# Optimization experiments

Measured on AMD Instinct MI355X. Metric: run time of the kernel, lower is better.

Reference implementation:

```python
import jax, jax.numpy as jnp
import numpy as np

B, S, DIM, H = 8, 1024, 768, 12
HD = DIM // H  # head_dim = 64
SCALE = HD ** -0.5


def setup_inputs() -> dict:
    key = jax.random.key(0)
    ks = jax.random.split(key, 9)
    std = DIM ** -0.5
    x = jax.random.normal(ks[0], (B, S, DIM), dtype=jnp.float32)
    Wq = jax.random.normal(ks[1], (DIM, DIM), dtype=jnp.float32) * std
    bq = jax.random.normal(ks[2], (DIM,), dtype=jnp.float32) * 0.01
    Wk = jax.random.normal(ks[3], (DIM, DIM), dtype=jnp.float32) * std
    bk = jax.random.normal(ks[4], (DIM,), dtype=jnp.float32) * 0.01
    Wv = jax.random.normal(ks[5], (DIM, DIM), dtype=jnp.float32) * std
    bv = jax.random.normal(ks[6], (DIM,), dtype=jnp.float32) * 0.01
    Wp = jax.random.normal(ks[7], (DIM, DIM), dtype=jnp.float32) * std
    bp = jax.random.normal(ks[8], (DIM,), dtype=jnp.float32) * 0.01
    return {"x": x, "Wq": Wq, "bq": bq, "Wk": Wk, "bk": bk,
            "Wv": Wv, "bv": bv, "Wp": Wp, "bp": bp}


def _split_heads(t):
    # [b, s, (n d)] -> [b, n, s, d]
    b, s, _ = t.shape
    return t.reshape(b, s, H, HD).transpose(0, 2, 1, 3)


def reference(x, Wq, bq, Wk, bk, Wv, bv, Wp, bp):
    q = _split_heads(x @ Wq + bq)
    k = _split_heads(x @ Wk + bk)
    v = _split_heads(x @ Wv + bv)
    attn = jnp.einsum('bnqd,bnkd->bnqk', q, k) * SCALE
    attn = jax.nn.softmax(attn, axis=-1)
    o = jnp.einsum('bnqk,bnkd->bnqd', attn, v)
    o = o.transpose(0, 2, 1, 3).reshape(x.shape[0], x.shape[1], DIM)
    return o @ Wp + bp
```

## Files before the change

kernel.cpp:

```cpp
#include <hip/hip_runtime.h>
#include <hip/hip_bf16.h>
#include <cstdint>

#define B_    8
#define S_    1024
#define DIM_  768
#define H_    12
#define HD_   64
#define QL2S_ 0.1803368801111204f

typedef __attribute__((ext_vector_type(8))) __bf16 bf16x8;
typedef __attribute__((ext_vector_type(4))) float  f32x4;

__device__ __forceinline__ short f2bf(float f) {
  union { float f; uint32_t u; } a;
  a.f = f;
  uint32_t u = a.u;
  uint32_t r = (u + 0x7FFFu + ((u >> 16) & 1u)) >> 16;
  return (short)r;
}

__device__ __forceinline__ float exp2a(float x) {
  float r;
  asm("v_exp_f32 %0, %1\n\ts_nop 1" : "=v"(r) : "v"(x));
  return r;
}

__device__ __forceinline__ uint32_t cvtpk(float a, float b) {
  uint32_t r;
  asm("v_cvt_pk_bf16_f32 %0, %1, %2" : "=v"(r) : "v"(a), "v"(b));
  return r;
}

__device__ __forceinline__ void gll16(const void* g, void* l) {
  __builtin_amdgcn_global_load_lds((const __attribute__((address_space(1))) void*)g,
                                   (__attribute__((address_space(3))) void*)l, 16, 0, 0);
}

__device__ __forceinline__ int swz(int row, int col) {
  return row * 128 + ((((col >> 3) ^ (row & 7)) & 7) << 4) + ((col & 7) << 1);
}

__global__ __launch_bounds__(256) void k_prep(const float* __restrict__ x,
                                              const float* __restrict__ W0,
                                              const float* __restrict__ W1,
                                              const float* __restrict__ W2,
                                              const float* __restrict__ W3,
                                              short* __restrict__ xb,
                                              short* o0, short* o1,
                                              short* o2, short* o3) {
  const int tx = threadIdx.x, ty = threadIdx.y;
  if (blockIdx.z == 4) {
    const int tid = ty * 32 + tx;
    int i = (blockIdx.y * 24 + blockIdx.x) * 256 + tid;
    const int n4 = 8192 * 768 / 4;
    const int nthr = 24 * 24 * 256;
    for (; i < n4; i += nthr) {
      const float4 v = ((const float4*)x)[i];
      short4 o;
      o.x = f2bf(v.x); o.y = f2bf(v.y); o.z = f2bf(v.z); o.w = f2bf(v.w);
      ((short4*)xb)[i] = o;
    }
    return;
  }
  const float* in = blockIdx.z == 0 ? W0 : blockIdx.z == 1 ? W1 : blockIdx.z == 2 ? W2 : W3;
  short* out = blockIdx.z == 0 ? o0 : blockIdx.z == 1 ? o1 : blockIdx.z == 2 ? o2 : o3;
  __shared__ float tile[32][33];
  const int bx = blockIdx.x * 32, by = blockIdx.y * 32;
#pragma unroll
  for (int j = 0; j < 32; j += 8)
    tile[ty + j][tx] = in[(size_t)(by + ty + j) * DIM_ + bx + tx];
  __syncthreads();
#pragma unroll
  for (int j = 0; j < 32; j += 8)
    out[(size_t)(bx + ty + j) * DIM_ + by + tx] = f2bf(tile[tx][ty + j]);
}

template <int MODE, bool QS>
__device__ __forceinline__ void gemm_body(char* smem,
                                          const short* __restrict__ A,
                                          const short* __restrict__ Bt,
                                          const float* __restrict__ bias,
                                          void* __restrict__ out,
                                          int bm, int bn) {
  char* As = smem;
  char* Bs = smem + 32768;
  const int tid = threadIdx.x;
  const int l = tid & 63, w = tid >> 6;
  const int hi = l >> 4, lo = l & 15;
  const int wr = w >> 1, wc = w & 1;

  auto stageA = [&](int ks, int bo) {
#pragma unroll
    for (int i = 0; i < 4; ++i) {
      const int gl = i * 256 + tid;
      const int row = gl >> 3;
      const int g = (gl & 7) ^ (row & 7);
      gll16(A + (size_t)(bm * 128 + row) * DIM_ + ks * 64 + g * 8, As + bo + gl * 16);
    }
  };
  auto stageB = [&](int ks, int bo) {
#pragma unroll
    for (int i = 0; i < 4; ++i) {
      const int gl = i * 256 + tid;
      const int row = gl >> 3;
      const int g = (gl & 7) ^ (row & 7);
      gll16(Bt + (size_t)(bn * 128 + row) * DIM_ + ks * 64 + g * 8, Bs + bo + gl * 16);
    }
  };

  f32x4 acc[4][4];
  const f32x4 zz = {0.f, 0.f, 0.f, 0.f};
#pragma unroll
  for (int m = 0; m < 4; ++m)
#pragma unroll
    for (int n = 0; n < 4; ++n) acc[m][n] = zz;

  stageA(0, 0);
  stageB(0, 0);
  __syncthreads();

  for (int ks = 0; ks < 12; ++ks) {
    const int cu = (ks & 1) << 14;
    if (ks < 11) { stageA(ks + 1, cu ^ 16384); stageB(ks + 1, cu ^ 16384); }
#pragma unroll
    for (int kk = 0; kk < 2; ++kk) {
      bf16x8 a[4], b[4];
#pragma unroll
      for (int m = 0; m < 4; ++m)
        a[m] = *(const bf16x8*)(As + cu + swz(wr * 64 + m * 16 + lo, kk * 32 + hi * 8));
#pragma unroll
      for (int n = 0; n < 4; ++n)
        b[n] = *(const bf16x8*)(Bs + cu + swz(wc * 64 + n * 16 + lo, kk * 32 + hi * 8));
#pragma unroll
      for (int m = 0; m < 4; ++m)
#pragma unroll
        for (int n = 0; n < 4; ++n)
          acc[m][n] = __builtin_amdgcn_mfma_f32_16x16x32_bf16(a[m], b[n], acc[m][n], 0, 0, 0);
    }
    __syncthreads();
  }

#pragma unroll
  for (int m = 0; m < 4; ++m) {
#pragma unroll
    for (int n = 0; n < 4; ++n) {
#pragma unroll
      for (int r = 0; r < 4; ++r) {
        const int R = bm * 128 + wr * 64 + m * 16 + hi * 4 + r;
        const int C = bn * 128 + wc * 64 + n * 16 + lo;
        float v = acc[m][n][r] + bias[MODE == 1 ? R : C];
        if (QS) v *= QL2S_;
        if (MODE == 0) {
          ((short*)out)[((size_t)((R >> 10) * H_ + (C >> 6)) * S_ + (R & 1023)) * HD_ + (C & 63)] = f2bf(v);
        } else if (MODE == 1) {
          ((short*)out)[((size_t)((C >> 10) * H_ + (R >> 6)) * HD_ + (R & 63)) * S_ + (C & 1023)] = f2bf(v);
        } else {
          ((float*)out)[(size_t)R * DIM_ + C] = v;
        }
      }
    }
  }
}

__global__ __launch_bounds__(256, 2) void k_gemm_qkv(const short* __restrict__ xb,
                                                     const short* __restrict__ WqT,
                                                     const short* __restrict__ WkT,
                                                     const short* __restrict__ WvT,
                                                     const float* __restrict__ bq,
                                                     const float* __restrict__ bk,
                                                     const float* __restrict__ bv,
                                                     short* qo, short* ko, short* vo) {
  __shared__ alignas(16) char smem[65536];
  if (blockIdx.z == 0)
    gemm_body<0, true>(smem, xb, WqT, bq, qo, blockIdx.x, blockIdx.y);
  else if (blockIdx.z == 1)
    gemm_body<0, false>(smem, xb, WkT, bk, ko, blockIdx.x, blockIdx.y);
  else
    gemm_body<1, false>(smem, WvT, xb, bv, vo, blockIdx.y, blockIdx.x);
}

__global__ __launch_bounds__(256, 2) void k_gemm_proj(const short* __restrict__ A,
                                                      const short* __restrict__ Bt,
                                                      const float* __restrict__ bias,
                                                      float* out) {
  __shared__ alignas(16) char smem[65536];
  gemm_body<2, false>(smem, A, Bt, bias, out, blockIdx.y, blockIdx.x);
}

__global__ __launch_bounds__(256, 3) void k_attn(const short* __restrict__ qw,
                                                 const short* __restrict__ kw,
                                                 const short* __restrict__ vtw,
                                                 short* __restrict__ ow) {
  __shared__ alignas(16) char smem[49152];
  char* Kb = smem;
  char* Vb = smem + 16384;
  char* Ps = smem + 32768;
  const int tid = threadIdx.x;
  const int l = tid & 63, w = tid >> 6;
  const int hi = l >> 4, lo = l & 15;
  const int qt = blockIdx.x / 96;
  const int bh = blockIdx.x % 96;

  const short* qg = qw  + (size_t)bh * (S_ * HD_) + (qt * 128) * HD_;
  const short* kg = kw  + (size_t)bh * (S_ * HD_);
  const short* vg = vtw + (size_t)bh * (S_ * HD_);

  auto stage = [&](int T, int bufo) {
#pragma unroll
    for (int i = 0; i < 2; ++i) {
      const int gl = i * 256 + tid;
      const int row = gl >> 3;
      const int g = (gl & 7) ^ (row & 7);
      gll16(kg + (T * 64 + row) * 64 + g * 8, Kb + bufo + gl * 16);
    }
#pragma unroll
    for (int i = 0; i < 2; ++i) {
      const int gl = i * 256 + tid;
      const int row = gl >> 3;
      const int g = (gl & 7) ^ (row & 7);
      gll16(vg + row * 1024 + T * 64 + g * 8, Vb + bufo + gl * 16);
    }
  };

  bf16x8 aQ[2][2];
#pragma unroll
  for (int m = 0; m < 2; ++m)
#pragma unroll
    for (int kk = 0; kk < 2; ++kk)
      aQ[m][kk] = *(const bf16x8*)(qg + (w * 32 + m * 16 + lo) * HD_ + kk * 32 + hi * 8);

  f32x4 o_acc[2][4];
  const f32x4 zz = {0.f, 0.f, 0.f, 0.f};
#pragma unroll
  for (int m = 0; m < 2; ++m)
#pragma unroll
    for (int db = 0; db < 4; ++db) o_acc[m][db] = zz;
  float lsum[2] = {0.f, 0.f};

  stage(0, 0);
  __syncthreads();

  for (int t = 0; t < 16; ++t) {
    const int cu = (t & 1) << 13;
    if (t < 15) stage(t + 1, cu ^ 8192);

    f32x4 sacc[2][4];
#pragma unroll
    for (int m = 0; m < 2; ++m)
#pragma unroll
      for (int nb = 0; nb < 4; ++nb) sacc[m][nb] = zz;
    __builtin_amdgcn_s_setprio(1);
#pragma unroll
    for (int kk = 0; kk < 2; ++kk) {
#pragma unroll
      for (int nb = 0; nb < 4; ++nb) {
        const bf16x8 bK = *(const bf16x8*)(Kb + cu + swz(nb * 16 + lo, kk * 32 + hi * 8));
#pragma unroll
        for (int m = 0; m < 2; ++m)
          sacc[m][nb] = __builtin_amdgcn_mfma_f32_16x16x32_bf16(bK, aQ[m][kk], sacc[m][nb], 0, 0, 0);
      }
    }
    __builtin_amdgcn_s_setprio(0);

#pragma unroll
    for (int m = 0; m < 2; ++m) {
#pragma unroll
      for (int nb = 0; nb < 4; ++nb) {
        const float p0 = exp2a(sacc[m][nb][0] - 1.0f);
        const float p1 = exp2a(sacc[m][nb][1] - 1.0f);
        const float p2 = exp2a(sacc[m][nb][2] - 1.0f);
        const float p3 = exp2a(sacc[m][nb][3] - 1.0f);
        lsum[m] += (p0 + p1) + (p2 + p3);
        uint2 pk;
        pk.x = cvtpk(p0, p1);
        pk.y = cvtpk(p2, p3);
        *(uint2*)(Ps + swz(w * 32 + m * 16 + lo, nb * 16 + hi * 4)) = pk;
      }
    }
    asm volatile("s_waitcnt lgkmcnt(0)" ::: "memory");
    __builtin_amdgcn_sched_barrier(0);

    __builtin_amdgcn_s_setprio(1);
#pragma unroll
    for (int kk = 0; kk < 2; ++kk) {
      bf16x8 aP[2];
#pragma unroll
      for (int m = 0; m < 2; ++m)
        aP[m] = *(const bf16x8*)(Ps + swz(w * 32 + m * 16 + lo, kk * 32 + hi * 8));
#pragma unroll
      for (int db = 0; db < 4; ++db) {
        const bf16x8 bV = *(const bf16x8*)(Vb + cu + swz(db * 16 + lo, kk * 32 + hi * 8));
#pragma unroll
        for (int m = 0; m < 2; ++m)
          o_acc[m][db] = __builtin_amdgcn_mfma_f32_16x16x32_bf16(aP[m], bV, o_acc[m][db], 0, 0, 0);
      }
    }
    __builtin_amdgcn_s_setprio(0);

    __syncthreads();
  }

  float lF[2];
#pragma unroll
  for (int m = 0; m < 2; ++m) {
    float s = lsum[m];
    s += __shfl_xor(s, 16, 64);
    s += __shfl_xor(s, 32, 64);
    lF[m] = s;
  }
  const int b = bh / H_, h = bh % H_;
#pragma unroll
  for (int m = 0; m < 2; ++m) {
#pragma unroll
    for (int r = 0; r < 4; ++r) {
      const float lr = __shfl(lF[m], hi * 4 + r, 64);
      const float inv = 1.0f / lr;
      const int sg = qt * 128 + w * 32 + m * 16 + hi * 4 + r;
#pragma unroll
      for (int db = 0; db < 4; ++db)
        ow[((size_t)(b * S_ + sg)) * DIM_ + h * HD_ + db * 16 + lo] = f2bf(o_acc[m][db][r] * inv);
    }
  }
}

extern "C" void kernel_launch(void* const* d_in, const int* in_sizes, int n_in,
                              void* d_out, int out_size, void* d_ws, size_t ws_size,
                              hipStream_t stream) {
  const float* x  = (const float*)d_in[0];
  const float* Wq = (const float*)d_in[1];
  const float* bq = (const float*)d_in[2];
  const float* Wk = (const float*)d_in[3];
  const float* bk = (const float*)d_in[4];
  const float* Wv = (const float*)d_in[5];
  const float* bv = (const float*)d_in[6];
  const float* Wp = (const float*)d_in[7];
  const float* bp = (const float*)d_in[8];

  char* ws = (char*)d_ws;
  size_t off = 0;
  auto alloc = [&](size_t bytes) {
    char* p = ws + off;
    off += (bytes + 255) & ~(size_t)255;
    return p;
  };
  short* xb  = (short*)alloc((size_t)8192 * 768 * 2);
  short* WqT = (short*)alloc((size_t)768 * 768 * 2);
  short* WkT = (short*)alloc((size_t)768 * 768 * 2);
  short* WvT = (short*)alloc((size_t)768 * 768 * 2);
  short* WpT = (short*)alloc((size_t)768 * 768 * 2);
  short* qwv = (short*)alloc((size_t)96 * 1024 * 64 * 2);
  short* kwv = (short*)alloc((size_t)96 * 1024 * 64 * 2);
  short* vtw = (short*)alloc((size_t)96 * 1024 * 64 * 2);
  short* owv = (short*)alloc((size_t)8192 * 768 * 2);

  dim3 tb(32, 8), tg(24, 24, 5);
  k_prep<<<tg, tb, 0, stream>>>(x, Wq, Wk, Wv, Wp, xb, WqT, WkT, WvT, WpT);

  k_gemm_qkv<<<dim3(64, 6, 3), 256, 0, stream>>>(xb, WqT, WkT, WvT, bq, bk, bv, qwv, kwv, vtw);

  k_attn<<<B_ * H_ * (S_ / 128), 256, 0, stream>>>(qwv, kwv, vtw, owv);

  k_gemm_proj<<<dim3(6, 64), 256, 0, stream>>>(owv, WpT, bp, (float*)d_out);
}
```

Measured before the change: 100.6 us.

## Keep attention probabilities in registers and feed PV via 16x16x16 MFMA

The exponentiated scores are packed straight into bf16x4 register operands and used as the A operand of 16x16x16 bf16 MFMAs. This removes the LDS round-trip for P: the shared-memory store, the lgkmcnt wait and the reload. LDS per block drops from 48 KB to 32 KB and the occupancy hint rises from 3 to 4 blocks. The cost is twice as many smaller-K MFMA instructions, narrower 8-byte V reads, and compiler-generated bf16 conversions in place of the packed convert instruction.

```diff
diff --git a/kernel.cpp b/kernel.cpp
--- a/kernel.cpp
+++ b/kernel.cpp
@@ -10,6 +10,8 @@
 #define QL2S_ 0.1803368801111204f
 
 typedef __attribute__((ext_vector_type(8))) __bf16 bf16x8;
+typedef __attribute__((ext_vector_type(4))) __bf16 bf16x4;
+typedef __attribute__((ext_vector_type(4))) short i16x4;
 typedef __attribute__((ext_vector_type(4))) float  f32x4;
 
 __device__ __forceinline__ short f2bf(float f) {
@@ -26,10 +28,14 @@
   return r;
 }
 
-__device__ __forceinline__ uint32_t cvtpk(float a, float b) {
-  uint32_t r;
-  asm("v_cvt_pk_bf16_f32 %0, %1, %2" : "=v"(r) : "v"(a), "v"(b));
-  return r;
+__device__ __forceinline__ f32x4 mfma16(bf16x4 a, bf16x4 b, f32x4 c) {
+#if __has_builtin(__builtin_amdgcn_mfma_f32_16x16x16_bf16)
+  return __builtin_amdgcn_mfma_f32_16x16x16_bf16(a, b, c, 0, 0, 0);
+#else
+  union { bf16x4 h; i16x4 s; } ua, ub;
+  ua.h = a; ub.h = b;
+  return __builtin_amdgcn_mfma_f32_16x16x16bf16_1k(ua.s, ub.s, c, 0, 0, 0);
+#endif
 }
 
 __device__ __forceinline__ void gll16(const void* g, void* l) {
@@ -188,14 +194,13 @@
   gemm_body<2, false>(smem, A, Bt, bias, out, blockIdx.y, blockIdx.x);
 }
 
-__global__ __launch_bounds__(256, 3) void k_attn(const short* __restrict__ qw,
+__global__ __launch_bounds__(256, 4) void k_attn(const short* __restrict__ qw,
                                                  const short* __restrict__ kw,
                                                  const short* __restrict__ vtw,
                                                  short* __restrict__ ow) {
-  __shared__ alignas(16) char smem[49152];
+  __shared__ alignas(16) char smem[32768];
   char* Kb = smem;
   char* Vb = smem + 16384;
-  char* Ps = smem + 32768;
   const int tid = threadIdx.x;
   const int l = tid & 63, w = tid >> 6;
   const int hi = l >> 4, lo = l & 15;
@@ -264,39 +269,28 @@
     __builtin_amdgcn_s_setprio(0);
 
 #pragma unroll
-    for (int m = 0; m < 2; ++m) {
-#pragma unroll
-      for (int nb = 0; nb < 4; ++nb) {
+    for (int nb = 0; nb < 4; ++nb) {
+      bf16x4 pa[2];
+#pragma unroll
+      for (int m = 0; m < 2; ++m) {
         const float p0 = exp2a(sacc[m][nb][0] - 1.0f);
         const float p1 = exp2a(sacc[m][nb][1] - 1.0f);
         const float p2 = exp2a(sacc[m][nb][2] - 1.0f);
         const float p3 = exp2a(sacc[m][nb][3] - 1.0f);
         lsum[m] += (p0 + p1) + (p2 + p3);
-        uint2 pk;
-        pk.x = cvtpk(p0, p1);
-        pk.y = cvtpk(p2, p3);
-        *(uint2*)(Ps + swz(w * 32 + m * 16 + lo, nb * 16 + hi * 4)) = pk;
+        pa[m][0] = (__bf16)p0;
+        pa[m][1] = (__bf16)p1;
+        pa[m][2] = (__bf16)p2;
+        pa[m][3] = (__bf16)p3;
       }
-    }
-    asm volatile("s_waitcnt lgkmcnt(0)" ::: "memory");
-    __builtin_amdgcn_sched_barrier(0);
-
-    __builtin_amdgcn_s_setprio(1);
-#pragma unroll
-    for (int kk = 0; kk < 2; ++kk) {
-      bf16x8 aP[2];
-#pragma unroll
-      for (int m = 0; m < 2; ++m)
-        aP[m] = *(const bf16x8*)(Ps + swz(w * 32 + m * 16 + lo, kk * 32 + hi * 8));
 #pragma unroll
       for (int db = 0; db < 4; ++db) {
-        const bf16x8 bV = *(const bf16x8*)(Vb + cu + swz(db * 16 + lo, kk * 32 + hi * 8));
+        const bf16x4 bV = *(const bf16x4*)(Vb + cu + swz(db * 16 + lo, nb * 16 + hi * 4));
 #pragma unroll
         for (int m = 0; m < 2; ++m)
-          o_acc[m][db] = __builtin_amdgcn_mfma_f32_16x16x32_bf16(aP[m], bV, o_acc[m][db], 0, 0, 0);
+          o_acc[m][db] = mfma16(pa[m], bV, o_acc[m][db]);
       }
     }
-    __builtin_amdgcn_s_setprio(0);
 
     __syncthreads();
   }
```

New measurement: 101.9 us. No clear change (+1.3%).

## Halve GEMM K-step to 32 and pack 128-row tiles as two 64-row halves

Applied to the files above, without the earlier changes.

The GEMM body now stages K-slices of 32 instead of 64, halving LDS use from 64 KB to 32 KB per block and doubling the number of K iterations to 24. Each staged 64-byte-wide row now holds two 64-row halves of the 128-row tile, and each warp reads its own half through a changed swizzle index. Launch bounds rise from 2 to 4 blocks per SM so more waves can hide load latency. The cost is twice as many barriers per tile and fewer MFMAs between syncs, with tighter register limits that may cause spills.

```diff
diff --git a/kernel.cpp b/kernel.cpp
--- a/kernel.cpp
+++ b/kernel.cpp
@@ -84,28 +84,28 @@
                                           void* __restrict__ out,
                                           int bm, int bn) {
   char* As = smem;
-  char* Bs = smem + 32768;
+  char* Bs = smem + 16384;
   const int tid = threadIdx.x;
   const int l = tid & 63, w = tid >> 6;
   const int hi = l >> 4, lo = l & 15;
   const int wr = w >> 1, wc = w & 1;
 
-  auto stageA = [&](int ks, int bo) {
-#pragma unroll
-    for (int i = 0; i < 4; ++i) {
+  auto stage = [&](int ks, int bo) {
+#pragma unroll
+    for (int i = 0; i < 2; ++i) {
       const int gl = i * 256 + tid;
-      const int row = gl >> 3;
-      const int g = (gl & 7) ^ (row & 7);
-      gll16(A + (size_t)(bm * 128 + row) * DIM_ + ks * 64 + g * 8, As + bo + gl * 16);
-    }
-  };
-  auto stageB = [&](int ks, int bo) {
-#pragma unroll
-    for (int i = 0; i < 4; ++i) {
+      const int row64 = gl >> 3;
+      const int gs = (gl & 7) ^ (row64 & 7);
+      gll16(A + (size_t)(bm * 128 + (gs >> 2) * 64 + row64) * DIM_ + ks * 32 + (gs & 3) * 8,
+            As + bo + gl * 16);
+    }
+#pragma unroll
+    for (int i = 0; i < 2; ++i) {
       const int gl = i * 256 + tid;
-      const int row = gl >> 3;
-      const int g = (gl & 7) ^ (row & 7);
-      gll16(Bt + (size_t)(bn * 128 + row) * DIM_ + ks * 64 + g * 8, Bs + bo + gl * 16);
+      const int row64 = gl >> 3;
+      const int gs = (gl & 7) ^ (row64 & 7);
+      gll16(Bt + (size_t)(bn * 128 + (gs >> 2) * 64 + row64) * DIM_ + ks * 32 + (gs & 3) * 8,
+            Bs + bo + gl * 16);
     }
   };
 
@@ -116,28 +116,24 @@
 #pragma unroll
     for (int n = 0; n < 4; ++n) acc[m][n] = zz;
 
-  stageA(0, 0);
-  stageB(0, 0);
+  stage(0, 0);
   __syncthreads();
 
-  for (int ks = 0; ks < 12; ++ks) {
-    const int cu = (ks & 1) << 14;
-    if (ks < 11) { stageA(ks + 1, cu ^ 16384); stageB(ks + 1, cu ^ 16384); }
-#pragma unroll
-    for (int kk = 0; kk < 2; ++kk) {
-      bf16x8 a[4], b[4];
-#pragma unroll
-      for (int m = 0; m < 4; ++m)
-        a[m] = *(const bf16x8*)(As + cu + swz(wr * 64 + m * 16 + lo, kk * 32 + hi * 8));
+  for (int ks = 0; ks < 24; ++ks) {
+    const int cu = (ks & 1) << 13;
+    if (ks < 23) stage(ks + 1, cu ^ 8192);
+    bf16x8 a[4], b[4];
+#pragma unroll
+    for (int m = 0; m < 4; ++m)
+      a[m] = *(const bf16x8*)(As + cu + swz(m * 16 + lo, wr * 32 + hi * 8));
+#pragma unroll
+    for (int n = 0; n < 4; ++n)
+      b[n] = *(const bf16x8*)(Bs + cu + swz(n * 16 + lo, wc * 32 + hi * 8));
+#pragma unroll
+    for (int m = 0; m < 4; ++m)
 #pragma unroll
       for (int n = 0; n < 4; ++n)
-        b[n] = *(const bf16x8*)(Bs + cu + swz(wc * 64 + n * 16 + lo, kk * 32 + hi * 8));
-#pragma unroll
-      for (int m = 0; m < 4; ++m)
-#pragma unroll
-        for (int n = 0; n < 4; ++n)
-          acc[m][n] = __builtin_amdgcn_mfma_f32_16x16x32_bf16(a[m], b[n], acc[m][n], 0, 0, 0);
-    }
+        acc[m][n] = __builtin_amdgcn_mfma_f32_16x16x32_bf16(a[m], b[n], acc[m][n], 0, 0, 0);
     __syncthreads();
   }
 
@@ -163,7 +159,7 @@
   }
 }
 
-__global__ __launch_bounds__(256, 2) void k_gemm_qkv(const short* __restrict__ xb,
+__global__ __launch_bounds__(256, 4) void k_gemm_qkv(const short* __restrict__ xb,
                                                      const short* __restrict__ WqT,
                                                      const short* __restrict__ WkT,
                                                      const short* __restrict__ WvT,
@@ -171,7 +167,7 @@
                                                      const float* __restrict__ bk,
                                                      const float* __restrict__ bv,
                                                      short* qo, short* ko, short* vo) {
-  __shared__ alignas(16) char smem[65536];
+  __shared__ alignas(16) char smem[32768];
   if (blockIdx.z == 0)
     gemm_body<0, true>(smem, xb, WqT, bq, qo, blockIdx.x, blockIdx.y);
   else if (blockIdx.z == 1)
@@ -180,11 +176,11 @@
     gemm_body<1, false>(smem, WvT, xb, bv, vo, blockIdx.y, blockIdx.x);
 }
 
-__global__ __launch_bounds__(256, 2) void k_gemm_proj(const short* __restrict__ A,
+__global__ __launch_bounds__(256, 4) void k_gemm_proj(const short* __restrict__ A,
                                                       const short* __restrict__ Bt,
                                                       const float* __restrict__ bias,
                                                       float* out) {
-  __shared__ alignas(16) char smem[65536];
+  __shared__ alignas(16) char smem[32768];
   gemm_body<2, false>(smem, A, Bt, bias, out, blockIdx.y, blockIdx.x);
 }
 
```

New measurement: 112.9 us. 12.3% more time.
